# Performance work log

Measured on AMD Instinct MI355X. Metric: run time of the kernel, lower is better.

## Reference

```python
import jax, jax.numpy as jnp
import numpy as np

SEQ, B, CIN, H, K = 2048, 16, 512, 512, 2

def setup_inputs() -> dict:
    key = jax.random.key(0)
    k1, k2, k3 = jax.random.split(key, 3)
    x = jax.random.normal(k1, (SEQ, B, CIN), dtype=jnp.float32)
    W = jax.random.normal(k2, (3 * H, CIN, K), dtype=jnp.float32) * (1.0 / np.sqrt(CIN * K))
    b = jax.random.normal(k3, (3 * H,), dtype=jnp.float32) * 0.01
    return {"x": x, "W": W, "b": b}

def _qrnn_fo(x, W, b):
    # x: (T, B, Cin) -> conv input (B, Cin, T), causal left pad of K-1 zeros
    xb = jnp.transpose(x, (1, 2, 0))
    g = jax.lax.conv_general_dilated(
        xb, W, window_strides=(1,), padding=[(K - 1, 0)],
        dimension_numbers=("NCH", "OIH", "NCH"))
    g = g + b[None, :, None]
    g = jnp.transpose(g, (2, 0, 1))  # (T, B, 3H)
    zg, fg, og = jnp.split(g, 3, axis=-1)
    z = jnp.tanh(zg)
    f = jax.nn.sigmoid(fg)
    o = jax.nn.sigmoid(og)

    def step(c, gates_t):
        zt, ft, ot = gates_t
        c = ft * c + (1.0 - ft) * zt
        h = c * ot
        return c, h

    c0 = jnp.zeros((B, H), dtype=x.dtype)
    c_last, hs = jax.lax.scan(step, c0, (z, f, o))
    return hs, c_last

def reference(x, W, b):
    hs, c_last = _qrnn_fo(x, W, b)
    h_last = hs[-1]
    return hs, h_last[None, :], c_last[None, :]
```

## Files before the change

### kernel.cpp

```cpp
#include <hip/hip_runtime.h>

#define SEQ   2048
#define BATCH 16
#define CINCH 512
#define HDIM  512
#define NDIM  1536
#define TBM   (SEQ*BATCH)
#define KRED  1024
#define NCH   256
#define CHL   8
#define NCOL  8192

typedef unsigned short ushort_t;
typedef __bf16 bf16x8 __attribute__((ext_vector_type(8)));
typedef unsigned short u16x8 __attribute__((ext_vector_type(8)));
typedef float f32x4 __attribute__((ext_vector_type(4)));

__device__ __forceinline__ float bf2f(ushort_t u) {
    return __uint_as_float(((unsigned int)u) << 16);
}
__device__ __forceinline__ ushort_t f2bf(float x) {
    unsigned int u = __float_as_uint(x);
    unsigned int r = u + 0x7fffu + ((u >> 16) & 1u);
    return (ushort_t)(r >> 16);
}

#define CAST_BLK 8196
#define RPK_BLK  6144
__global__ void prep_kernel(const float* __restrict__ x, ushort_t* __restrict__ xb,
                            const float* __restrict__ W, ushort_t* __restrict__ wb) {
    if (blockIdx.x < CAST_BLK) {
        int e = (blockIdx.x * 256 + threadIdx.x) * 8;
        u16x8 r;
        if (e < BATCH * CINCH) {
            r = (u16x8){0, 0, 0, 0, 0, 0, 0, 0};
        } else {
            const float* p = x + (e - BATCH * CINCH);
            float4 v0 = *(const float4*)p;
            float4 v1 = *(const float4*)(p + 4);
            r[0] = f2bf(v0.x); r[1] = f2bf(v0.y); r[2] = f2bf(v0.z); r[3] = f2bf(v0.w);
            r[4] = f2bf(v1.x); r[5] = f2bf(v1.y); r[6] = f2bf(v1.z); r[7] = f2bf(v1.w);
        }
        *(u16x8*)(xb + e) = r;
    } else {
        int i = (blockIdx.x - CAST_BLK) * 256 + threadIdx.x;
        int o  = i >> 10;
        int r  = i & 1023;
        int k  = r >> 9;
        int ci = r & 511;
        wb[i] = f2bf(W[o * 1024 + ci * 2 + k]);
    }
}

__device__ __forceinline__ void load_lds_16B(const ushort_t* g, ushort_t* l) {
    auto* gp = reinterpret_cast<const __attribute__((address_space(1))) unsigned int*>(
        reinterpret_cast<uintptr_t>(g));
    auto* lp = reinterpret_cast<__attribute__((address_space(3))) unsigned int*>(
        reinterpret_cast<uintptr_t>(l));
    __builtin_amdgcn_global_load_lds(gp, lp, 16, 0, 0);
}

__global__ __launch_bounds__(256) void gemm_gates_kernel(
    const ushort_t* __restrict__ xb, const ushort_t* __restrict__ wb,
    const float* __restrict__ bias,
    ushort_t* __restrict__ zb, ushort_t* __restrict__ fb, ushort_t* __restrict__ ob) {

    __shared__ ushort_t smem[2 * 128 * 64];
    ushort_t* As = smem;
    ushort_t* Bs = smem + 128 * 64;

    const int tid  = threadIdx.x;
    const int w    = tid >> 6;
    const int lane = tid & 63;
    const int quad = lane >> 4;
    const int l15  = lane & 15;
    const int wm   = w & 1;
    const int wn   = w >> 1;
    const int mBase = blockIdx.x * 128;
    const int nBase = blockIdx.y * 128;

    const int srow = lane >> 3;
    const int scb  = lane & 7;

    f32x4 acc[4][4];
#pragma unroll
    for (int i = 0; i < 4; ++i)
#pragma unroll
        for (int j = 0; j < 4; ++j)
            acc[i][j] = (f32x4){0.f, 0.f, 0.f, 0.f};

    for (int kt = 0; kt < 16; ++kt) {
        __syncthreads();
        const long aOff = (kt < 8) ? (long)kt * 64 : (long)16 * 512 + (long)(kt - 8) * 64;
#pragma unroll
        for (int i = 0; i < 4; ++i) {
            const int row = w * 32 + i * 8 + srow;
            const int cbd = scb ^ (row & 7);
            const ushort_t* ga = xb + (long)(mBase + row) * 512 + aOff + cbd * 8;
            load_lds_16B(ga, &As[(w * 32 + i * 8) * 64]);
            const ushort_t* gb = wb + (long)(nBase + row) * 1024 + kt * 64 + cbd * 8;
            load_lds_16B(gb, &Bs[(w * 32 + i * 8) * 64]);
        }
        __syncthreads();

#pragma unroll
        for (int ks = 0; ks < 2; ++ks) {
            bf16x8 af[4], bfr[4];
            const int cbd = ks * 4 + quad;
#pragma unroll
            for (int mt = 0; mt < 4; ++mt) {
                int ml  = wm * 64 + mt * 16 + l15;
                int off = ml * 64 + ((cbd ^ (ml & 7)) * 8);
                af[mt] = __builtin_bit_cast(bf16x8, *(const u16x8*)(&As[off]));
            }
#pragma unroll
            for (int nt = 0; nt < 4; ++nt) {
                int nl  = wn * 64 + nt * 16 + l15;
                int off = nl * 64 + ((cbd ^ (nl & 7)) * 8);
                bfr[nt] = __builtin_bit_cast(bf16x8, *(const u16x8*)(&Bs[off]));
            }
#pragma unroll
            for (int mt = 0; mt < 4; ++mt)
#pragma unroll
                for (int nt = 0; nt < 4; ++nt)
                    acc[mt][nt] = __builtin_amdgcn_mfma_f32_16x16x32_bf16(
                        af[mt], bfr[nt], acc[mt][nt], 0, 0, 0);
        }
    }

    const int gate = nBase >> 9;
    const int hb   = nBase & 511;

    __syncthreads();
#pragma unroll
    for (int nt = 0; nt < 4; ++nt) {
        const int n_local = wn * 64 + nt * 16 + l15;
        const float bv = bias[nBase + n_local];
#pragma unroll
        for (int mt = 0; mt < 4; ++mt) {
#pragma unroll
            for (int r = 0; r < 4; ++r) {
                const int m_local = wm * 64 + mt * 16 + quad * 4 + r;
                float g = acc[mt][nt][r] + bv;
                float a;
                if (gate == 0) {
                    float e = __expf(-2.f * fabsf(g));
                    float t = (1.f - e) / (1.f + e);
                    a = copysignf(t, g);
                } else {
                    a = 1.f / (1.f + __expf(-g));
                }
                const int phys = ((n_local >> 3) ^ (m_local & 7)) * 8 + (n_local & 7);
                smem[m_local * 128 + phys] = f2bf(a);
            }
        }
    }
    __syncthreads();

    ushort_t* outp = (gate == 0) ? zb : (gate == 1) ? fb : ob;
#pragma unroll
    for (int s = 0; s < 8; ++s) {
        const int m_local = w * 32 + s * 4 + quad;
        const int blk = l15 ^ (m_local & 7);
        u16x8 v = *(const u16x8*)(&smem[m_local * 128 + blk * 8]);
        *(u16x8*)(outp + (long)(mBase + m_local) * 512 + hb + l15 * 8) = v;
    }
}

__global__ __launch_bounds__(256) void scan_compose(
    const ushort_t* __restrict__ zb, const ushort_t* __restrict__ fb,
    float* __restrict__ Acomp, float* __restrict__ Bcomp) {
    const int ch   = blockIdx.x >> 2;
    const int col0 = (((blockIdx.x & 3) * 256) + threadIdx.x) * 8;
    const long base = (long)ch * CHL * NCOL + col0;

    u16x8 zc[CHL], fc[CHL];
#pragma unroll
    for (int t = 0; t < CHL; ++t) {
        zc[t] = *(const u16x8*)(zb + base + (long)t * NCOL);
        fc[t] = *(const u16x8*)(fb + base + (long)t * NCOL);
    }
    float A[8], Bv[8];
#pragma unroll
    for (int j = 0; j < 8; ++j) { A[j] = 1.f; Bv[j] = 0.f; }
#pragma unroll
    for (int t = 0; t < CHL; ++t) {
#pragma unroll
        for (int j = 0; j < 8; ++j) {
            float f = bf2f(fc[t][j]), z = bf2f(zc[t][j]);
            Bv[j] = f * Bv[j] + (1.f - f) * z;
            A[j] *= f;
        }
    }
    f32x4 a0 = {A[0], A[1], A[2], A[3]}, a1 = {A[4], A[5], A[6], A[7]};
    f32x4 b0 = {Bv[0], Bv[1], Bv[2], Bv[3]}, b1 = {Bv[4], Bv[5], Bv[6], Bv[7]};
    *(f32x4*)(Acomp + (long)ch * NCOL + col0)     = a0;
    *(f32x4*)(Acomp + (long)ch * NCOL + col0 + 4) = a1;
    *(f32x4*)(Bcomp + (long)ch * NCOL + col0)     = b0;
    *(f32x4*)(Bcomp + (long)ch * NCOL + col0 + 4) = b1;
}

__global__ void scan_prefix(const float* __restrict__ Acomp,
                            const float* __restrict__ Bcomp,
                            float* __restrict__ Cin) {
    const int col = blockIdx.x * 256 + threadIdx.x;
    float c = 0.f;
#pragma unroll 8
    for (int ch = 0; ch < NCH; ++ch) {
        Cin[ch * NCOL + col] = c;
        c = Acomp[ch * NCOL + col] * c + Bcomp[ch * NCOL + col];
    }
}

__global__ __launch_bounds__(256) void scan_apply(
    const ushort_t* __restrict__ zb, const ushort_t* __restrict__ fb,
    const ushort_t* __restrict__ ob, const float* __restrict__ Cin,
    float* __restrict__ out) {
    const int ch   = blockIdx.x >> 2;
    const int col0 = (((blockIdx.x & 3) * 256) + threadIdx.x) * 8;
    const long base = (long)ch * CHL * NCOL + col0;

    u16x8 zc[CHL], fc[CHL], oc[CHL];
#pragma unroll
    for (int t = 0; t < CHL; ++t) {
        zc[t] = *(const u16x8*)(zb + base + (long)t * NCOL);
        fc[t] = *(const u16x8*)(fb + base + (long)t * NCOL);
        oc[t] = *(const u16x8*)(ob + base + (long)t * NCOL);
    }
    float c[8], h[8];
    f32x4 c0 = *(const f32x4*)(Cin + (long)ch * NCOL + col0);
    f32x4 c1 = *(const f32x4*)(Cin + (long)ch * NCOL + col0 + 4);
    c[0] = c0[0]; c[1] = c0[1]; c[2] = c0[2]; c[3] = c0[3];
    c[4] = c1[0]; c[5] = c1[1]; c[6] = c1[2]; c[7] = c1[3];

#pragma unroll
    for (int t = 0; t < CHL; ++t) {
#pragma unroll
        for (int j = 0; j < 8; ++j) {
            float f = bf2f(fc[t][j]), z = bf2f(zc[t][j]), o = bf2f(oc[t][j]);
            c[j] = f * c[j] + (1.f - f) * z;
            h[j] = c[j] * o;
        }
        f32x4 h0 = {h[0], h[1], h[2], h[3]}, h1 = {h[4], h[5], h[6], h[7]};
        *(f32x4*)(out + base + (long)t * NCOL)     = h0;
        *(f32x4*)(out + base + (long)t * NCOL + 4) = h1;
    }
    if (ch == NCH - 1) {
        f32x4 h0 = {h[0], h[1], h[2], h[3]}, h1 = {h[4], h[5], h[6], h[7]};
        f32x4 cc0 = {c[0], c[1], c[2], c[3]}, cc1 = {c[4], c[5], c[6], c[7]};
        *(f32x4*)(out + (long)SEQ * NCOL + col0)            = h0;
        *(f32x4*)(out + (long)SEQ * NCOL + col0 + 4)        = h1;
        *(f32x4*)(out + (long)SEQ * NCOL + NCOL + col0)     = cc0;
        *(f32x4*)(out + (long)SEQ * NCOL + NCOL + col0 + 4) = cc1;
    }
}

extern "C" void kernel_launch(void* const* d_in, const int* in_sizes, int n_in,
                              void* d_out, int out_size, void* d_ws, size_t ws_size,
                              hipStream_t stream) {
    const float* x  = (const float*)d_in[0];
    const float* W  = (const float*)d_in[1];
    const float* bi = (const float*)d_in[2];
    float* out = (float*)d_out;

    char* ws = (char*)d_ws;
    const size_t xbN = (size_t)(TBM + BATCH) * CINCH;
    const size_t wbN = (size_t)NDIM * KRED;
    const size_t gN  = (size_t)TBM * HDIM;
    ushort_t* xb = (ushort_t*)ws;
    ushort_t* wb = (ushort_t*)(ws + xbN * 2);
    ushort_t* zb = (ushort_t*)(ws + xbN * 2 + wbN * 2);
    ushort_t* fb = zb + gN;
    ushort_t* ob = fb + gN;
    float* Acomp = (float*)ws;
    float* Bcomp = Acomp + NCH * NCOL;
    float* Cin   = Bcomp + NCH * NCOL;

    prep_kernel<<<CAST_BLK + RPK_BLK, 256, 0, stream>>>(x, xb, W, wb);
    dim3 ggrid(TBM / 128, NDIM / 128);
    gemm_gates_kernel<<<ggrid, 256, 0, stream>>>(xb, wb, bi, zb, fb, ob);
    scan_compose<<<NCH * 4, 256, 0, stream>>>(zb, fb, Acomp, Bcomp);
    scan_prefix<<<NCOL / 256, 256, 0, stream>>>(Acomp, Bcomp, Cin);
    scan_apply<<<NCH * 4, 256, 0, stream>>>(zb, fb, ob, Cin, out);
}
```

Before: 308.2 us.

## Fuse chunk scan composition into GEMM epilogue via interleaved z/f weight tiles

Reorders the packed weight rows so each GEMM N-tile holds matching z and f columns side by side, and vectorizes the weight repack with float4 loads. The GEMM epilogue then computes each 128-row chunk's (A,B) scan composition from the activations in shared memory and combines the two warp halves through an LDS scratch buffer, which removes the separate scan_compose kernel and its reread of z/f. The fused path is taken only when the workspace is large enough, and it adds epilogue work, an extra barrier and extra LDS use to the GEMM.

```diff
diff --git a/kernel.cpp b/kernel.cpp
--- a/kernel.cpp
+++ b/kernel.cpp
@@ -26,7 +26,7 @@
 }
 
 #define CAST_BLK 8196
-#define RPK_BLK  6144
+#define RPK_BLK  384
 __global__ void prep_kernel(const float* __restrict__ x, ushort_t* __restrict__ xb,
                             const float* __restrict__ W, ushort_t* __restrict__ wb) {
     if (blockIdx.x < CAST_BLK) {
@@ -43,12 +43,23 @@
         }
         *(u16x8*)(xb + e) = r;
     } else {
-        int i = (blockIdx.x - CAST_BLK) * 256 + threadIdx.x;
-        int o  = i >> 10;
-        int r  = i & 1023;
-        int k  = r >> 9;
-        int ci = r & 511;
-        wb[i] = f2bf(W[o * 1024 + ci * 2 + k]);
+        int idx = (blockIdx.x - CAST_BLK) * 256 + threadIdx.x;
+        int nn = idx >> 6;
+        int c0 = (idx & 63) * 8;
+        int jn = nn >> 7, p = nn & 127;
+        int src = (jn < 8) ? ((p >> 6) * 512 + jn * 64 + (p & 63)) : nn;
+        const float* wp = W + (long)src * 1024 + c0 * 2;
+        float4 q0 = *(const float4*)(wp);
+        float4 q1 = *(const float4*)(wp + 4);
+        float4 q2 = *(const float4*)(wp + 8);
+        float4 q3 = *(const float4*)(wp + 12);
+        u16x8 ev, od;
+        ev[0] = f2bf(q0.x); od[0] = f2bf(q0.y); ev[1] = f2bf(q0.z); od[1] = f2bf(q0.w);
+        ev[2] = f2bf(q1.x); od[2] = f2bf(q1.y); ev[3] = f2bf(q1.z); od[3] = f2bf(q1.w);
+        ev[4] = f2bf(q2.x); od[4] = f2bf(q2.y); ev[5] = f2bf(q2.z); od[5] = f2bf(q2.w);
+        ev[6] = f2bf(q3.x); od[6] = f2bf(q3.y); ev[7] = f2bf(q3.z); od[7] = f2bf(q3.w);
+        *(u16x8*)(wb + (long)nn * 1024 + c0)       = ev;
+        *(u16x8*)(wb + (long)nn * 1024 + 512 + c0) = od;
     }
 }
 
@@ -63,9 +74,11 @@
 __global__ __launch_bounds__(256) void gemm_gates_kernel(
     const ushort_t* __restrict__ xb, const ushort_t* __restrict__ wb,
     const float* __restrict__ bias,
-    ushort_t* __restrict__ zb, ushort_t* __restrict__ fb, ushort_t* __restrict__ ob) {
+    ushort_t* __restrict__ zb, ushort_t* __restrict__ fb, ushort_t* __restrict__ ob,
+    float* __restrict__ acomp, float* __restrict__ bcomp) {
 
     __shared__ ushort_t smem[2 * 128 * 64];
+    __shared__ float escratch[16 * 128];
     ushort_t* As = smem;
     ushort_t* Bs = smem + 128 * 64;
 
@@ -128,14 +141,17 @@
         }
     }
 
-    const int gate = nBase >> 9;
-    const int hb   = nBase & 511;
+    const bool zfTile = (nBase < 1024);
+    const int  jzf    = nBase >> 7;
+    const bool isTanh = zfTile && (wn == 0);
 
     __syncthreads();
 #pragma unroll
     for (int nt = 0; nt < 4; ++nt) {
         const int n_local = wn * 64 + nt * 16 + l15;
-        const float bv = bias[nBase + n_local];
+        const int bsrc = zfTile ? (wn * 512 + jzf * 64 + (nt * 16 + l15))
+                                : (nBase + n_local);
+        const float bv = bias[bsrc];
 #pragma unroll
         for (int mt = 0; mt < 4; ++mt) {
 #pragma unroll
@@ -143,7 +159,7 @@
                 const int m_local = wm * 64 + mt * 16 + quad * 4 + r;
                 float g = acc[mt][nt][r] + bv;
                 float a;
-                if (gate == 0) {
+                if (isTanh) {
                     float e = __expf(-2.f * fabsf(g));
                     float t = (1.f - e) / (1.f + e);
                     a = copysignf(t, g);
@@ -157,13 +173,77 @@
     }
     __syncthreads();
 
-    ushort_t* outp = (gate == 0) ? zb : (gate == 1) ? fb : ob;
-#pragma unroll
-    for (int s = 0; s < 8; ++s) {
-        const int m_local = w * 32 + s * 4 + quad;
-        const int blk = l15 ^ (m_local & 7);
-        u16x8 v = *(const u16x8*)(&smem[m_local * 128 + blk * 8]);
-        *(u16x8*)(outp + (long)(mBase + m_local) * 512 + hb + l15 * 8) = v;
+    if (zfTile) {
+        const int l8 = lane >> 3;
+        const int cb = lane & 7;
+#pragma unroll
+        for (int s = 0; s < 4; ++s) {
+            const int m_local = w * 32 + s * 8 + l8;
+            const int px = cb ^ (m_local & 7);
+            u16x8 vz = *(const u16x8*)(&smem[m_local * 128 + px * 8]);
+            *(u16x8*)(zb + (long)(mBase + m_local) * 512 + jzf * 64 + cb * 8) = vz;
+            u16x8 vf = *(const u16x8*)(&smem[m_local * 128 + (8 + px) * 8]);
+            *(u16x8*)(fb + (long)(mBase + m_local) * 512 + jzf * 64 + cb * 8) = vf;
+        }
+    } else {
+        const int hb = nBase - 1024;
+#pragma unroll
+        for (int s = 0; s < 8; ++s) {
+            const int m_local = w * 32 + s * 4 + quad;
+            const int blk = l15 ^ (m_local & 7);
+            u16x8 v = *(const u16x8*)(&smem[m_local * 128 + blk * 8]);
+            *(u16x8*)(ob + (long)(mBase + m_local) * 512 + hb + l15 * 8) = v;
+        }
+    }
+
+    float aH[4][4], bH[4][4];
+    if (acomp && zfTile && wn == 1) {
+#pragma unroll
+        for (int nt = 0; nt < 4; ++nt)
+#pragma unroll
+            for (int r = 0; r < 4; ++r) { aH[nt][r] = 1.f; bH[nt][r] = 0.f; }
+#pragma unroll
+        for (int mt = 0; mt < 4; ++mt) {
+#pragma unroll
+            for (int nt = 0; nt < 4; ++nt) {
+                const int zc = nt * 16 + l15;
+                const int zb3 = zc >> 3, zlow = zc & 7;
+#pragma unroll
+                for (int r = 0; r < 4; ++r) {
+                    const int m_local = wm * 64 + mt * 16 + quad * 4 + r;
+                    const int px = zb3 ^ (m_local & 7);
+                    float zv = bf2f(smem[m_local * 128 + px * 8 + zlow]);
+                    float fv = bf2f(smem[m_local * 128 + (8 + px) * 8 + zlow]);
+                    bH[nt][r] = fv * bH[nt][r] + (1.f - fv) * zv;
+                    aH[nt][r] *= fv;
+                }
+            }
+        }
+        if (wm == 0) {
+#pragma unroll
+            for (int nt = 0; nt < 4; ++nt)
+#pragma unroll
+                for (int r = 0; r < 4; ++r) {
+                    escratch[(nt * 4 + r) * 128 + lane * 2]     = aH[nt][r];
+                    escratch[(nt * 4 + r) * 128 + lane * 2 + 1] = bH[nt][r];
+                }
+        }
+    }
+    __syncthreads();
+    if (acomp && zfTile && wn == 1 && wm == 1) {
+        const int ch = blockIdx.x;
+#pragma unroll
+        for (int nt = 0; nt < 4; ++nt)
+#pragma unroll
+            for (int r = 0; r < 4; ++r) {
+                float a0 = escratch[(nt * 4 + r) * 128 + lane * 2];
+                float b0 = escratch[(nt * 4 + r) * 128 + lane * 2 + 1];
+                float A  = aH[nt][r] * a0;
+                float Bv = aH[nt][r] * b0 + bH[nt][r];
+                const int col = (quad * 4 + r) * 512 + jzf * 64 + nt * 16 + l15;
+                acomp[(long)ch * NCOL + col] = A;
+                bcomp[(long)ch * NCOL + col] = Bv;
+            }
     }
 }
 
@@ -184,14 +264,13 @@
 #pragma unroll
     for (int j = 0; j < 8; ++j) { A[j] = 1.f; Bv[j] = 0.f; }
 #pragma unroll
-    for (int t = 0; t < CHL; ++t) {
+    for (int t = 0; t < CHL; ++t)
 #pragma unroll
         for (int j = 0; j < 8; ++j) {
             float f = bf2f(fc[t][j]), z = bf2f(zc[t][j]);
             Bv[j] = f * Bv[j] + (1.f - f) * z;
             A[j] *= f;
         }
-    }
     f32x4 a0 = {A[0], A[1], A[2], A[3]}, a1 = {A[4], A[5], A[6], A[7]};
     f32x4 b0 = {Bv[0], Bv[1], Bv[2], Bv[3]}, b1 = {Bv[4], Bv[5], Bv[6], Bv[7]};
     *(f32x4*)(Acomp + (long)ch * NCOL + col0)     = a0;
@@ -264,22 +343,37 @@
     float* out = (float*)d_out;
 
     char* ws = (char*)d_ws;
-    const size_t xbN = (size_t)(TBM + BATCH) * CINCH;
-    const size_t wbN = (size_t)NDIM * KRED;
-    const size_t gN  = (size_t)TBM * HDIM;
+    const size_t xbB = (size_t)(TBM + BATCH) * CINCH * 2;
+    const size_t wbB = (size_t)NDIM * KRED * 2;
+    const size_t gB  = (size_t)TBM * HDIM * 2;
+    const size_t abB = (size_t)NCH * NCOL * 4;
     ushort_t* xb = (ushort_t*)ws;
-    ushort_t* wb = (ushort_t*)(ws + xbN * 2);
-    ushort_t* zb = (ushort_t*)(ws + xbN * 2 + wbN * 2);
-    ushort_t* fb = zb + gN;
-    ushort_t* ob = fb + gN;
-    float* Acomp = (float*)ws;
-    float* Bcomp = Acomp + NCH * NCOL;
-    float* Cin   = Bcomp + NCH * NCOL;
+    ushort_t* wb = (ushort_t*)(ws + xbB);
+    ushort_t* zb = (ushort_t*)(ws + xbB + wbB);
+    ushort_t* fb = zb + (size_t)TBM * HDIM;
+    ushort_t* ob = fb + (size_t)TBM * HDIM;
+
+    const size_t needFused = xbB + wbB + 3 * gB + 2 * abB;
+    const bool fused = (ws_size >= needFused);
+
+    float *Acomp, *Bcomp, *Cin;
+    if (fused) {
+        Acomp = (float*)(ws + xbB + wbB + 3 * gB);
+        Bcomp = Acomp + (size_t)NCH * NCOL;
+        Cin   = (float*)ws;
+    } else {
+        Acomp = (float*)ws;
+        Bcomp = Acomp + (size_t)NCH * NCOL;
+        Cin   = Bcomp + (size_t)NCH * NCOL;
+    }
 
     prep_kernel<<<CAST_BLK + RPK_BLK, 256, 0, stream>>>(x, xb, W, wb);
     dim3 ggrid(TBM / 128, NDIM / 128);
-    gemm_gates_kernel<<<ggrid, 256, 0, stream>>>(xb, wb, bi, zb, fb, ob);
-    scan_compose<<<NCH * 4, 256, 0, stream>>>(zb, fb, Acomp, Bcomp);
+    gemm_gates_kernel<<<ggrid, 256, 0, stream>>>(xb, wb, bi, zb, fb, ob,
+                                                 fused ? Acomp : nullptr,
+                                                 fused ? Bcomp : nullptr);
+    if (!fused)
+        scan_compose<<<NCH * 4, 256, 0, stream>>>(zb, fb, Acomp, Bcomp);
     scan_prefix<<<NCOL / 256, 256, 0, stream>>>(Acomp, Bcomp, Cin);
     scan_apply<<<NCH * 4, 256, 0, stream>>>(zb, fb, ob, Cin, out);
 }
```

New measurement: 323.6 us. +5.0%, slower.
